# Performance work log

Hardware: AMD Instinct MI355X
Metric: run time of the kernel (lower is better)

Reference implementation:

```python
import jax, jax.numpy as jnp
import numpy as np

N_VOCAB = 50000
V_SUPPORT = 20000
D = 300
H = 512
B = 8192


def setup_inputs() -> dict:
    key = jax.random.key(0)
    ks = jax.random.split(key, 8)
    ws = jax.random.randint(ks[0], (B,), 0, N_VOCAB, dtype=jnp.int64 if jax.config.jax_enable_x64 else jnp.int32)
    cs = jax.random.randint(ks[1], (B,), 0, N_VOCAB, dtype=ws.dtype)
    vectors = jax.random.normal(ks[2], (N_VOCAB, D), dtype=jnp.float32)
    W1 = jax.random.normal(ks[3], (D, H), dtype=jnp.float32) * (1.0 / np.sqrt(D))
    b1 = jnp.zeros((H,), dtype=jnp.float32)
    W2 = jax.random.normal(ks[4], (H, V_SUPPORT), dtype=jnp.float32) * (1.0 / np.sqrt(H))
    b2 = jnp.zeros((V_SUPPORT,), dtype=jnp.float32)
    vector_to_support = jax.random.randint(ks[5], (N_VOCAB,), 0, V_SUPPORT, dtype=ws.dtype)
    return {"ws": ws, "cs": cs, "vectors": vectors, "W1": W1, "b1": b1,
            "W2": W2, "b2": b2, "vector_to_support": vector_to_support}


def reference(ws, cs, vectors, W1, b1, W2, b2, vector_to_support):
    # embedding lookup of context vectors: [B, D]
    v_c = vectors[cs]
    # FeedForward: Linear -> ReLU -> Linear, then LogSoftmax over support
    h = jax.nn.relu(v_c @ W1 + b1)            # [B, H]
    logits = h @ W2 + b2                       # [B, V]
    logp = jax.nn.log_softmax(logits, axis=-1) # [B, V]
    # map target word (vocab index) -> support index, gather per-row logprob.
    # Original does outputs.T[idx].diag() (O(B^2)); the fused equivalent is a
    # per-row gather: logp[arange(B), idx].
    w_sup = vector_to_support[ws]              # [B]
    logprobs = jnp.take_along_axis(logp, w_sup[:, None], axis=-1)[:, 0]
    return -logprobs                            # [B] NLL per example
```

## Files before the change

kernel.cpp:

```cpp
#include <hip/hip_runtime.h>
#include <hip/hip_bf16.h>
#include <hip/hip_fp8.h>
#include <math.h>


typedef __bf16 bf16x8 __attribute__((ext_vector_type(8)));
typedef float f32x4 __attribute__((ext_vector_type(4)));
typedef int i32x4 __attribute__((ext_vector_type(4)));
typedef int i32x8 __attribute__((ext_vector_type(8)));

#define B_N 8192
#define D_N 300
#define K1K 320
#define H_N 512
#define V_N 20000
#define V_PAD 20480
#define NSPLIT 16
#define SPLIT_V 1280
#define NCH 40
#define ROWS_BLK 128
#define CHUNK_BYTES 16384

#define OFF_PART (8388608u)
#define OFF_W1T  (OFF_PART + 16u*8192u*8u)
#define OFF_B2L  (OFF_W1T + 512u*320u*2u)
#define OFF_H8   (OFF_B2L + 20480u*4u)
#define OFF_W2T8 (OFF_H8 + 8192u*512u)

#define SCALE1 0x7F7F7F7F
#define LOG2E  1.4426950408889634f

__device__ inline unsigned short f2bf(float f) {
  __hip_bfloat16 h = __float2bfloat16(f);
  return *reinterpret_cast<unsigned short*>(&h);
}

__device__ inline unsigned char f2fp8(float f) {
  __hip_fp8_e4m3 q(f);
  return (unsigned char)q.__x;
}

__device__ inline unsigned int pk4_fp8(float a, float b, float c, float d) {
#if __has_builtin(__builtin_amdgcn_cvt_pk_fp8_f32)
  int v = 0;
  v = __builtin_amdgcn_cvt_pk_fp8_f32(a, b, v, false);
  v = __builtin_amdgcn_cvt_pk_fp8_f32(c, d, v, true);
  return (unsigned int)v;
#else
  return (unsigned int)f2fp8(a) | ((unsigned int)f2fp8(b) << 8) |
         ((unsigned int)f2fp8(c) << 16) | ((unsigned int)f2fp8(d) << 24);
#endif
}

__device__ inline float fp82f(unsigned char b) {
  __hip_fp8_e4m3 q; q.__x = b;
  return (float)q;
}

__device__ __forceinline__ void gl16(const void* g, void* l) {
  __builtin_amdgcn_global_load_lds(
      (const __attribute__((address_space(1))) void*)g,
      (__attribute__((address_space(3))) void*)l, 16, 0, 0);
}

__global__ __launch_bounds__(256) void kprep(
    const float* __restrict__ W2, unsigned long long* __restrict__ W2T8u,
    const float* __restrict__ W1, unsigned int* __restrict__ W1Tu,
    const float* __restrict__ b2, float* __restrict__ b2l)
{
  __shared__ float tile[64][65];
  const int bid = blockIdx.x;
  const int tid = threadIdx.x;

  if (bid < 2560) {
    const int n0 = (bid >> 3) * 64;
    const int k0 = (bid & 7) * 64;
    #pragma unroll
    for (int it = 0; it < 4; ++it) {
      int idx = it * 256 + tid;
      int i = idx >> 4;
      int j4 = (idx & 15) * 4;
      const float* src = &W2[(size_t)(k0 + i) * V_N + n0 + j4];
      float4 v = make_float4(0.f, 0.f, 0.f, 0.f);
      if (n0 + j4 + 3 < V_N) {
        v = *(const float4*)src;
      } else {
        if (n0 + j4 + 0 < V_N) v.x = src[0];
        if (n0 + j4 + 1 < V_N) v.y = src[1];
        if (n0 + j4 + 2 < V_N) v.z = src[2];
        if (n0 + j4 + 3 < V_N) v.w = src[3];
      }
      tile[i][j4 + 0] = v.x; tile[i][j4 + 1] = v.y;
      tile[i][j4 + 2] = v.z; tile[i][j4 + 3] = v.w;
    }
    __syncthreads();
    #pragma unroll
    for (int it = 0; it < 2; ++it) {
      int idx = it * 256 + tid;
      int nl = idx >> 3;
      int g8 = (idx & 7) * 8;
      int n = n0 + nl;
      unsigned int lo = pk4_fp8(tile[g8 + 0][nl], tile[g8 + 1][nl],
                                tile[g8 + 2][nl], tile[g8 + 3][nl]);
      unsigned int hi = pk4_fp8(tile[g8 + 4][nl], tile[g8 + 5][nl],
                                tile[g8 + 6][nl], tile[g8 + 7][nl]);
      unsigned long long pack = ((unsigned long long)hi << 32) | lo;
      unsigned kk = (unsigned)(k0 + g8);
      unsigned off = ((unsigned)n * 512u + (kk ^ (((unsigned)n & 15u) << 4)));
      W2T8u[off >> 3] = pack;
    }
  } else if (bid < 2600) {
    const int idx0 = bid - 2560;
    const int n0 = (idx0 & 7) * 64;
    const int k0 = (idx0 >> 3) * 64;
    #pragma unroll
    for (int it = 0; it < 16; ++it) {
      int idx = it * 256 + tid;
      int i = idx >> 6;
      int j = idx & 63;
      float v = 0.f;
      if (k0 + i < D_N) v = W1[(size_t)(k0 + i) * H_N + n0 + j];
      tile[i][j] = v;
    }
    __syncthreads();
    #pragma unroll
    for (int it = 0; it < 8; ++it) {
      int idx = it * 256 + tid;
      int nl = idx >> 5;
      int k = (idx & 31) * 2;
      unsigned int lo = f2bf(tile[k][nl]);
      unsigned int hi = f2bf(tile[k + 1][nl]);
      W1Tu[((size_t)(n0 + nl) * K1K + k0 + k) >> 1] = (hi << 16) | lo;
    }
  } else {
    int i = (bid - 2600) * 256 + tid;
    if (i < V_PAD) b2l[i] = (i < V_N) ? b2[i] * LOG2E : -3.0e37f;
  }
}

__global__ __launch_bounds__(256) void k1_hidden(
    const int* __restrict__ cs, const float* __restrict__ vectors,
    const unsigned short* __restrict__ W1T,
    const float* __restrict__ b1, unsigned char* __restrict__ h8Out)
{
  __shared__ __align__(16) unsigned short vca[16][328];
  __shared__ int rowIdx[16];
  const int tid = threadIdx.x;
  const int lane = tid & 63;
  const int w = tid >> 6;
  const int l15 = lane & 15;
  const int l4 = lane >> 4;
  const int r0 = blockIdx.x * 16;
  if (tid < 16) rowIdx[tid] = cs[r0 + tid];
  __syncthreads();
  for (int task = tid; task < 16 * 82; task += 256) {
    const int r = task & 15;
    const int g = task >> 4;
    const int k = g * 4;
    float4 v = make_float4(0.f, 0.f, 0.f, 0.f);
    if (k + 3 < D_N)
      v = *(const float4*)(vectors + (size_t)rowIdx[r] * D_N + k);
    ushort4 pk;
    pk.x = f2bf(v.x); pk.y = f2bf(v.y); pk.z = f2bf(v.z); pk.w = f2bf(v.w);
    *(ushort4*)&vca[r][k] = pk;
  }
  __syncthreads();

  bf16x8 afr[10];
  #pragma unroll
  for (int t = 0; t < 10; ++t)
    afr[t] = *(const bf16x8*)&vca[l15][t * 32 + l4 * 8];

  f32x4 acc[8];
  #pragma unroll
  for (int ct = 0; ct < 8; ++ct) acc[ct] = (f32x4){0.f, 0.f, 0.f, 0.f};

  #pragma unroll
  for (int t = 0; t < 10; ++t) {
    #pragma unroll
    for (int ct = 0; ct < 8; ++ct) {
      const int n = w * 128 + ct * 16 + l15;
      bf16x8 bfr = *(const bf16x8*)(W1T + (size_t)n * K1K + t * 32 + l4 * 8);
      acc[ct] = __builtin_amdgcn_mfma_f32_16x16x32_bf16(afr[t], bfr, acc[ct], 0, 0, 0);
    }
  }

  #pragma unroll
  for (int ct = 0; ct < 8; ++ct) {
    const int n = w * 128 + ct * 16 + l15;
    const float bb = b1[n];
    #pragma unroll
    for (int r = 0; r < 4; ++r) {
      const int row = r0 + l4 * 4 + r;
      h8Out[(size_t)row * H_N + n] = f2fp8(fmaxf(acc[ct][r] + bb, 0.f));
    }
  }
}

__device__ __forceinline__ void stage_chunk(const char* g, char* l, int tid) {
  #pragma unroll
  for (int it = 0; it < 4; ++it) {
    const unsigned o = (unsigned)tid * 16 + it * 4096;
    gl16(g + o, l + o);
  }
}

__global__ __launch_bounds__(256, 4) void k3_fused(
    const unsigned char* __restrict__ h8,
    const char* __restrict__ W2T8,
    const float* __restrict__ b2l,
    float2* __restrict__ partOut)
{
  __shared__ __align__(16) char smB[2 * CHUNK_BYTES];
  __shared__ float b2s[SPLIT_V];
  const int tid = threadIdx.x;
  const int lane = tid & 63;
  const int w = tid >> 6;
  const int l15 = lane & 15;
  const int l4 = lane >> 4;
  const int s = blockIdx.x & 15;
  const int rb = blockIdx.x >> 4;
  const int r0 = rb * ROWS_BLK + w * 32;
  const char* gsplit = W2T8 + (size_t)s * SPLIT_V * 512;
  const int sCol = s * SPLIT_V;
  const int c0 = (rb * 7 + s * 3) % NCH;

  i32x8 afr[2][4];
  #pragma unroll
  for (int m = 0; m < 2; ++m) {
    const unsigned char* ap = h8 + (size_t)(r0 + m * 16 + l15) * H_N + l4 * 32;
    #pragma unroll
    for (int t = 0; t < 4; ++t) {
      i32x4 lo = *(const i32x4*)(ap + t * 128);
      i32x4 hi = *(const i32x4*)(ap + t * 128 + 16);
      afr[m][t] = __builtin_shufflevector(lo, hi, 0, 1, 2, 3, 4, 5, 6, 7);
    }
  }

  float s_run[8];
  #pragma unroll
  for (int ri = 0; ri < 8; ++ri) s_run[ri] = 0.f;

  for (int i = tid; i < SPLIT_V; i += 256) b2s[i] = b2l[sCol + i];

  stage_chunk(gsplit + (size_t)c0 * CHUNK_BYTES, smB, tid);

  const unsigned swz = (unsigned)l15 << 4;

  #pragma unroll 1
  for (int i = 0; i < NCH; ++i) {
    const int cc = (c0 + i >= NCH) ? (c0 + i - NCH) : (c0 + i);
    asm volatile("s_waitcnt vmcnt(0) lgkmcnt(0)" ::: "memory");
    __builtin_amdgcn_s_barrier();

    char* cur = smB + (i & 1) * CHUNK_BYTES;
    if (i + 1 < NCH) {
      const int cn = (cc + 1 >= NCH) ? 0 : (cc + 1);
      stage_chunk(gsplit + (size_t)cn * CHUNK_BYTES,
                  smB + ((i & 1) ^ 1) * CHUNK_BYTES, tid);
    }

    const float b2c0 = b2s[cc * 32 + l15];
    const float b2c1 = b2s[cc * 32 + 16 + l15];

    f32x4 acc[2][2];
    #pragma unroll
    for (int m = 0; m < 2; ++m)
      #pragma unroll
      for (int ct = 0; ct < 2; ++ct) acc[m][ct] = (f32x4){0.f, 0.f, 0.f, 0.f};

    #pragma unroll
    for (int t = 0; t < 4; ++t) {
      const char* bp = cur + l15 * 512;
      i32x4 lo = *(const i32x4*)(bp + (((unsigned)(t * 128 + l4 * 32)) ^ swz));
      i32x4 hi = *(const i32x4*)(bp + (((unsigned)(t * 128 + l4 * 32 + 16)) ^ swz));
      i32x8 bfr = __builtin_shufflevector(lo, hi, 0, 1, 2, 3, 4, 5, 6, 7);
      __builtin_amdgcn_s_setprio(1);
      acc[0][0] = __builtin_amdgcn_mfma_scale_f32_16x16x128_f8f6f4(
          afr[0][t], bfr, acc[0][0], 0, 0, 0, SCALE1, 0, SCALE1);
      acc[1][0] = __builtin_amdgcn_mfma_scale_f32_16x16x128_f8f6f4(
          afr[1][t], bfr, acc[1][0], 0, 0, 0, SCALE1, 0, SCALE1);
      __builtin_amdgcn_s_setprio(0);
    }

    #pragma unroll
    for (int t = 0; t < 4; ++t) {
      const char* bp = cur + (16 + l15) * 512;
      i32x4 lo = *(const i32x4*)(bp + (((unsigned)(t * 128 + l4 * 32)) ^ swz));
      i32x4 hi = *(const i32x4*)(bp + (((unsigned)(t * 128 + l4 * 32 + 16)) ^ swz));
      i32x8 bfr = __builtin_shufflevector(lo, hi, 0, 1, 2, 3, 4, 5, 6, 7);
      __builtin_amdgcn_s_setprio(1);
      acc[0][1] = __builtin_amdgcn_mfma_scale_f32_16x16x128_f8f6f4(
          afr[0][t], bfr, acc[0][1], 0, 0, 0, SCALE1, 0, SCALE1);
      acc[1][1] = __builtin_amdgcn_mfma_scale_f32_16x16x128_f8f6f4(
          afr[1][t], bfr, acc[1][1], 0, 0, 0, SCALE1, 0, SCALE1);
      __builtin_amdgcn_s_setprio(0);
      #pragma unroll
      for (int r2 = 0; r2 < 2; ++r2) {
        const int ri = t * 2 + r2;
        const int m_ = ri >> 2, r_ = ri & 3;
        s_run[ri] += __builtin_amdgcn_exp2f(fmaf(acc[m_][0][r_], LOG2E, b2c0));
      }
    }

    #pragma unroll
    for (int m = 0; m < 2; ++m)
      #pragma unroll
      for (int r = 0; r < 4; ++r)
        s_run[m * 4 + r] += __builtin_amdgcn_exp2f(fmaf(acc[m][1][r], LOG2E, b2c1));
  }

  #pragma unroll
  for (int m = 0; m < 2; ++m)
    #pragma unroll
    for (int r = 0; r < 4; ++r) {
      int ri = m * 4 + r;
      float sc = s_run[ri];
      #pragma unroll
      for (int k = 1; k < 16; k <<= 1) sc += __shfl_xor(sc, k);
      if (l15 == 0) {
        int grow = r0 + m * 16 + l4 * 4 + r;
        partOut[(size_t)s * B_N + grow] = make_float2(0.f, sc);
      }
    }
}

__global__ __launch_bounds__(256) void k45_final(
    const unsigned char* __restrict__ h8, const char* __restrict__ W2T8,
    const float* __restrict__ b2, const int* __restrict__ wsIdx,
    const int* __restrict__ v2s, const float2* __restrict__ part,
    float* __restrict__ out)
{
  const int row = blockIdx.x * 4 + (threadIdx.x >> 6);
  const int lane = threadIdx.x & 63;
  const int tc = v2s[wsIdx[row]];
  unsigned long long hv = *(const unsigned long long*)(h8 + (size_t)row * H_N + lane * 8);
  const unsigned off = ((unsigned)(lane * 8)) ^ (((unsigned)tc & 15u) << 4);
  unsigned long long wv = *(const unsigned long long*)(W2T8 + (size_t)tc * 512 + off);
  float sdot = 0.f;
  #pragma unroll
  for (int j = 0; j < 8; ++j)
    sdot += fp82f((unsigned char)(hv >> (8 * j))) * fp82f((unsigned char)(wv >> (8 * j)));
  #pragma unroll
  for (int k = 32; k >= 1; k >>= 1) sdot += __shfl_xor(sdot, k);
  if (lane == 0) {
    const float tgt = sdot + b2[tc];
    float S = 0.f;
    #pragma unroll
    for (int s = 0; s < NSPLIT; ++s) S += part[(size_t)s * B_N + row].y;
    out[row] = logf(S) - tgt;
  }
}

extern "C" void kernel_launch(void* const* d_in, const int* in_sizes, int n_in,
                              void* d_out, int out_size, void* d_ws, size_t ws_size,
                              hipStream_t stream) {
  const int*   wsIdx   = (const int*)d_in[0];
  const int*   cs      = (const int*)d_in[1];
  const float* vectors = (const float*)d_in[2];
  const float* W1      = (const float*)d_in[3];
  const float* b1      = (const float*)d_in[4];
  const float* W2      = (const float*)d_in[5];
  const float* b2      = (const float*)d_in[6];
  const int*   v2s     = (const int*)d_in[7];

  char* wsb = (char*)d_ws;
  float2* part = (float2*)(wsb + OFF_PART);
  unsigned short* W1T = (unsigned short*)(wsb + OFF_W1T);
  float*  b2l  = (float*)(wsb + OFF_B2L);
  unsigned char* h8   = (unsigned char*)(wsb + OFF_H8);
  char*   W2T8 = wsb + OFF_W2T8;
  float*  out  = (float*)d_out;

  hipLaunchKernelGGL(kprep, dim3(2680), dim3(256), 0, stream,
                     W2, (unsigned long long*)W2T8, W1, (unsigned int*)W1T, b2, b2l);
  hipLaunchKernelGGL(k1_hidden, dim3(B_N / 16), dim3(256), 0, stream, cs, vectors, W1T, b1, h8);
  hipLaunchKernelGGL(k3_fused, dim3((B_N / ROWS_BLK) * NSPLIT), dim3(256), 0, stream,
                     h8, W2T8, b2l, part);
  hipLaunchKernelGGL(k45_final, dim3(B_N / 4), dim3(256), 0, stream,
                     h8, W2T8, b2, wsIdx, v2s, part, out);
}
```

Measured before the change: 117.5 us.

## Load second half of W2 chunk directly from global in MFMA fragment layout

The prep kernel now also writes the second 16 columns of each 32-column W2 chunk into a fragment-ordered buffer, so the fused GEMM can load those B operands straight from global memory into registers. Only the first half of each chunk is staged through LDS, which halves the LDS staging buffer and the LDS traffic. The chunk start rotation per block is dropped. The cost is direct global loads on the critical path with less latency hiding, plus an extra write in prep. The new buffer sits at workspace offset 0, which may overlap other data there.

```diff
diff --git a/kernel.cpp b/kernel.cpp
--- a/kernel.cpp
+++ b/kernel.cpp
@@ -20,7 +20,9 @@
 #define NCH 40
 #define ROWS_BLK 128
 #define CHUNK_BYTES 16384
-
+#define STG_BYTES 8192
+
+#define OFF_W2F  0u
 #define OFF_PART (8388608u)
 #define OFF_W1T  (OFF_PART + 16u*8192u*8u)
 #define OFF_B2L  (OFF_W1T + 512u*320u*2u)
@@ -65,6 +67,7 @@
 
 __global__ __launch_bounds__(256) void kprep(
     const float* __restrict__ W2, unsigned long long* __restrict__ W2T8u,
+    unsigned long long* __restrict__ W2Fu,
     const float* __restrict__ W1, unsigned int* __restrict__ W1Tu,
     const float* __restrict__ b2, float* __restrict__ b2l)
 {
@@ -108,6 +111,14 @@
       unsigned kk = (unsigned)(k0 + g8);
       unsigned off = ((unsigned)n * 512u + (kk ^ (((unsigned)n & 15u) << 4)));
       W2T8u[off >> 3] = pack;
+      if (n & 16) {
+        unsigned sc = (unsigned)n >> 5;
+        unsigned t  = kk >> 7;
+        unsigned l4g = (kk >> 5) & 3;
+        unsigned lanei = l4g * 16 + ((unsigned)n & 15);
+        unsigned foff = (((sc * 4u + t) * 64u) + lanei) * 32u + (kk & 31u);
+        W2Fu[foff >> 3] = pack;
+      }
     }
   } else if (bid < 2600) {
     const int idx0 = bid - 2560;
@@ -197,9 +208,9 @@
   }
 }
 
-__device__ __forceinline__ void stage_chunk(const char* g, char* l, int tid) {
-  #pragma unroll
-  for (int it = 0; it < 4; ++it) {
+__device__ __forceinline__ void stage_half(const char* g, char* l, int tid) {
+  #pragma unroll
+  for (int it = 0; it < 2; ++it) {
     const unsigned o = (unsigned)tid * 16 + it * 4096;
     gl16(g + o, l + o);
   }
@@ -208,10 +219,11 @@
 __global__ __launch_bounds__(256, 4) void k3_fused(
     const unsigned char* __restrict__ h8,
     const char* __restrict__ W2T8,
+    const char* __restrict__ W2F,
     const float* __restrict__ b2l,
     float2* __restrict__ partOut)
 {
-  __shared__ __align__(16) char smB[2 * CHUNK_BYTES];
+  __shared__ __align__(16) char smB[2 * STG_BYTES];
   __shared__ float b2s[SPLIT_V];
   const int tid = threadIdx.x;
   const int lane = tid & 63;
@@ -222,8 +234,8 @@
   const int rb = blockIdx.x >> 4;
   const int r0 = rb * ROWS_BLK + w * 32;
   const char* gsplit = W2T8 + (size_t)s * SPLIT_V * 512;
+  const char* fsplit = W2F + (size_t)s * (NCH * 4 * 2048) + (size_t)lane * 32;
   const int sCol = s * SPLIT_V;
-  const int c0 = (rb * 7 + s * 3) % NCH;
 
   i32x8 afr[2][4];
   #pragma unroll
@@ -243,25 +255,22 @@
 
   for (int i = tid; i < SPLIT_V; i += 256) b2s[i] = b2l[sCol + i];
 
-  stage_chunk(gsplit + (size_t)c0 * CHUNK_BYTES, smB, tid);
+  stage_half(gsplit, smB, tid);
 
   const unsigned swz = (unsigned)l15 << 4;
 
   #pragma unroll 1
-  for (int i = 0; i < NCH; ++i) {
-    const int cc = (c0 + i >= NCH) ? (c0 + i - NCH) : (c0 + i);
+  for (int c = 0; c < NCH; ++c) {
     asm volatile("s_waitcnt vmcnt(0) lgkmcnt(0)" ::: "memory");
     __builtin_amdgcn_s_barrier();
 
-    char* cur = smB + (i & 1) * CHUNK_BYTES;
-    if (i + 1 < NCH) {
-      const int cn = (cc + 1 >= NCH) ? 0 : (cc + 1);
-      stage_chunk(gsplit + (size_t)cn * CHUNK_BYTES,
-                  smB + ((i & 1) ^ 1) * CHUNK_BYTES, tid);
-    }
-
-    const float b2c0 = b2s[cc * 32 + l15];
-    const float b2c1 = b2s[cc * 32 + 16 + l15];
+    char* cur = smB + (c & 1) * STG_BYTES;
+    if (c + 1 < NCH)
+      stage_half(gsplit + (size_t)(c + 1) * CHUNK_BYTES,
+                 smB + ((c & 1) ^ 1) * STG_BYTES, tid);
+
+    const float b2c0 = b2s[c * 32 + l15];
+    const float b2c1 = b2s[c * 32 + 16 + l15];
 
     f32x4 acc[2][2];
     #pragma unroll
@@ -285,9 +294,9 @@
 
     #pragma unroll
     for (int t = 0; t < 4; ++t) {
-      const char* bp = cur + (16 + l15) * 512;
-      i32x4 lo = *(const i32x4*)(bp + (((unsigned)(t * 128 + l4 * 32)) ^ swz));
-      i32x4 hi = *(const i32x4*)(bp + (((unsigned)(t * 128 + l4 * 32 + 16)) ^ swz));
+      const char* fb = fsplit + (size_t)(c * 4 + t) * 2048;
+      i32x4 lo = *(const i32x4*)(fb);
+      i32x4 hi = *(const i32x4*)(fb + 16);
       i32x8 bfr = __builtin_shufflevector(lo, hi, 0, 1, 2, 3, 4, 5, 6, 7);
       __builtin_amdgcn_s_setprio(1);
       acc[0][1] = __builtin_amdgcn_mfma_scale_f32_16x16x128_f8f6f4(
@@ -365,6 +374,7 @@
   const int*   v2s     = (const int*)d_in[7];
 
   char* wsb = (char*)d_ws;
+  char*   W2F  = wsb + OFF_W2F;
   float2* part = (float2*)(wsb + OFF_PART);
   unsigned short* W1T = (unsigned short*)(wsb + OFF_W1T);
   float*  b2l  = (float*)(wsb + OFF_B2L);
@@ -373,10 +383,11 @@
   float*  out  = (float*)d_out;
 
   hipLaunchKernelGGL(kprep, dim3(2680), dim3(256), 0, stream,
-                     W2, (unsigned long long*)W2T8, W1, (unsigned int*)W1T, b2, b2l);
+                     W2, (unsigned long long*)W2T8, (unsigned long long*)W2F,
+                     W1, (unsigned int*)W1T, b2, b2l);
   hipLaunchKernelGGL(k1_hidden, dim3(B_N / 16), dim3(256), 0, stream, cs, vectors, W1T, b1, h8);
   hipLaunchKernelGGL(k3_fused, dim3((B_N / ROWS_BLK) * NSPLIT), dim3(256), 0, stream,
-                     h8, W2T8, b2l, part);
+                     h8, W2T8, W2F, b2l, part);
   hipLaunchKernelGGL(k45_final, dim3(B_N / 4), dim3(256), 0, stream,
                      h8, W2T8, b2, wsIdx, v2s, part, out);
 }
```

Measured after the change: 124.7 us. +6.0%, slower.

## Overlap W2 conversion with hidden-layer compute and unroll chunk loop by two

Applied to the files above, without the earlier changes.

The prep work is split in two. A small kernel converts W1 and b2. A second kernel runs the hidden-layer computation and the large W2 transpose and FP8 pack in the same grid, so the two overlap and one launch boundary goes away. In the main fused kernel, the staggered per-block chunk start is removed and the chunk loop is manually unrolled by two with fixed double-buffer pointers, which drops the modulo and index arithmetic. The risk is that all blocks now read the same W2 chunks in the same order, which could concentrate memory traffic. The merged kernel also uses more shared memory per block.

```diff
diff --git a/kernel.cpp b/kernel.cpp
--- a/kernel.cpp
+++ b/kernel.cpp
@@ -63,18 +63,57 @@
       (__attribute__((address_space(3))) void*)l, 16, 0, 0);
 }
 
-__global__ __launch_bounds__(256) void kprep(
-    const float* __restrict__ W2, unsigned long long* __restrict__ W2T8u,
+__global__ __launch_bounds__(256) void kprep_a(
     const float* __restrict__ W1, unsigned int* __restrict__ W1Tu,
     const float* __restrict__ b2, float* __restrict__ b2l)
 {
   __shared__ float tile[64][65];
   const int bid = blockIdx.x;
   const int tid = threadIdx.x;
-
-  if (bid < 2560) {
-    const int n0 = (bid >> 3) * 64;
-    const int k0 = (bid & 7) * 64;
+  if (bid < 40) {
+    const int n0 = (bid & 7) * 64;
+    const int k0 = (bid >> 3) * 64;
+    #pragma unroll
+    for (int it = 0; it < 16; ++it) {
+      int idx = it * 256 + tid;
+      int i = idx >> 6;
+      int j = idx & 63;
+      float v = 0.f;
+      if (k0 + i < D_N) v = W1[(size_t)(k0 + i) * H_N + n0 + j];
+      tile[i][j] = v;
+    }
+    __syncthreads();
+    #pragma unroll
+    for (int it = 0; it < 8; ++it) {
+      int idx = it * 256 + tid;
+      int nl = idx >> 5;
+      int k = (idx & 31) * 2;
+      unsigned int lo = f2bf(tile[k][nl]);
+      unsigned int hi = f2bf(tile[k + 1][nl]);
+      W1Tu[((size_t)(n0 + nl) * K1K + k0 + k) >> 1] = (hi << 16) | lo;
+    }
+  } else {
+    int i = (bid - 40) * 256 + tid;
+    if (i < V_PAD) b2l[i] = (i < V_N) ? b2[i] * LOG2E : -3.0e37f;
+  }
+}
+
+__global__ __launch_bounds__(256) void kprep_b(
+    const int* __restrict__ cs, const float* __restrict__ vectors,
+    const unsigned short* __restrict__ W1T, const float* __restrict__ b1,
+    unsigned char* __restrict__ h8Out,
+    const float* __restrict__ W2, unsigned long long* __restrict__ W2T8u)
+{
+  __shared__ float tile[64][65];
+  __shared__ __align__(16) unsigned short vca[16][328];
+  __shared__ int rowIdx[16];
+  const int bid = blockIdx.x;
+  const int tid = threadIdx.x;
+
+  if (bid >= 512) {
+    const int wb = bid - 512;
+    const int n0 = (wb >> 3) * 64;
+    const int k0 = (wb & 7) * 64;
     #pragma unroll
     for (int it = 0; it < 4; ++it) {
       int idx = it * 256 + tid;
@@ -109,48 +148,14 @@
       unsigned off = ((unsigned)n * 512u + (kk ^ (((unsigned)n & 15u) << 4)));
       W2T8u[off >> 3] = pack;
     }
-  } else if (bid < 2600) {
-    const int idx0 = bid - 2560;
-    const int n0 = (idx0 & 7) * 64;
-    const int k0 = (idx0 >> 3) * 64;
-    #pragma unroll
-    for (int it = 0; it < 16; ++it) {
-      int idx = it * 256 + tid;
-      int i = idx >> 6;
-      int j = idx & 63;
-      float v = 0.f;
-      if (k0 + i < D_N) v = W1[(size_t)(k0 + i) * H_N + n0 + j];
-      tile[i][j] = v;
-    }
-    __syncthreads();
-    #pragma unroll
-    for (int it = 0; it < 8; ++it) {
-      int idx = it * 256 + tid;
-      int nl = idx >> 5;
-      int k = (idx & 31) * 2;
-      unsigned int lo = f2bf(tile[k][nl]);
-      unsigned int hi = f2bf(tile[k + 1][nl]);
-      W1Tu[((size_t)(n0 + nl) * K1K + k0 + k) >> 1] = (hi << 16) | lo;
-    }
-  } else {
-    int i = (bid - 2600) * 256 + tid;
-    if (i < V_PAD) b2l[i] = (i < V_N) ? b2[i] * LOG2E : -3.0e37f;
-  }
-}
-
-__global__ __launch_bounds__(256) void k1_hidden(
-    const int* __restrict__ cs, const float* __restrict__ vectors,
-    const unsigned short* __restrict__ W1T,
-    const float* __restrict__ b1, unsigned char* __restrict__ h8Out)
-{
-  __shared__ __align__(16) unsigned short vca[16][328];
-  __shared__ int rowIdx[16];
-  const int tid = threadIdx.x;
+    return;
+  }
+
   const int lane = tid & 63;
   const int w = tid >> 6;
   const int l15 = lane & 15;
   const int l4 = lane >> 4;
-  const int r0 = blockIdx.x * 16;
+  const int r0 = bid * 16;
   if (tid < 16) rowIdx[tid] = cs[r0 + tid];
   __syncthreads();
   for (int task = tid; task < 16 * 82; task += 256) {
@@ -204,6 +209,63 @@
     gl16(g + o, l + o);
   }
 }
+
+#define CHUNK_BODY(c, CUR, NXT, GUARD)                                         \
+  {                                                                            \
+    asm volatile("s_waitcnt vmcnt(0) lgkmcnt(0)" ::: "memory");                \
+    __builtin_amdgcn_s_barrier();                                              \
+    if (GUARD)                                                                 \
+      stage_chunk(gsplit + (size_t)((c) + 1) * CHUNK_BYTES, (NXT), tid);       \
+    const float b2c0 = b2s[(c) * 32 + l15];                                    \
+    const float b2c1 = b2s[(c) * 32 + 16 + l15];                               \
+    f32x4 acc[2][2];                                                           \
+    _Pragma("unroll")                                                          \
+    for (int m_ = 0; m_ < 2; ++m_)                                             \
+      _Pragma("unroll")                                                        \
+      for (int ct_ = 0; ct_ < 2; ++ct_)                                        \
+        acc[m_][ct_] = (f32x4){0.f, 0.f, 0.f, 0.f};                            \
+                                                    \
+    _Pragma("unroll")                                                          \
+    for (int t_ = 0; t_ < 4; ++t_) {                                           \
+      const char* bp = (CUR) + l15 * 512;                                      \
+      i32x4 lo = *(const i32x4*)(bp + (((unsigned)(t_*128 + l4*32)) ^ swz));   \
+      i32x4 hi = *(const i32x4*)(bp + (((unsigned)(t_*128 + l4*32 + 16)) ^ swz)); \
+      i32x8 bfr = __builtin_shufflevector(lo, hi, 0, 1, 2, 3, 4, 5, 6, 7);     \
+      __builtin_amdgcn_s_setprio(1);                                           \
+      acc[0][0] = __builtin_amdgcn_mfma_scale_f32_16x16x128_f8f6f4(            \
+          afr[0][t_], bfr, acc[0][0], 0, 0, 0, SCALE1, 0, SCALE1);             \
+      acc[1][0] = __builtin_amdgcn_mfma_scale_f32_16x16x128_f8f6f4(            \
+          afr[1][t_], bfr, acc[1][0], 0, 0, 0, SCALE1, 0, SCALE1);             \
+      __builtin_amdgcn_s_setprio(0);                                           \
+    }                                                                          \
+                          \
+    _Pragma("unroll")                                                          \
+    for (int t_ = 0; t_ < 4; ++t_) {                                           \
+      const char* bp = (CUR) + (16 + l15) * 512;                               \
+      i32x4 lo = *(const i32x4*)(bp + (((unsigned)(t_*128 + l4*32)) ^ swz));   \
+      i32x4 hi = *(const i32x4*)(bp + (((unsigned)(t_*128 + l4*32 + 16)) ^ swz)); \
+      i32x8 bfr = __builtin_shufflevector(lo, hi, 0, 1, 2, 3, 4, 5, 6, 7);     \
+      __builtin_amdgcn_s_setprio(1);                                           \
+      acc[0][1] = __builtin_amdgcn_mfma_scale_f32_16x16x128_f8f6f4(            \
+          afr[0][t_], bfr, acc[0][1], 0, 0, 0, SCALE1, 0, SCALE1);             \
+      acc[1][1] = __builtin_amdgcn_mfma_scale_f32_16x16x128_f8f6f4(            \
+          afr[1][t_], bfr, acc[1][1], 0, 0, 0, SCALE1, 0, SCALE1);             \
+      __builtin_amdgcn_s_setprio(0);                                           \
+      _Pragma("unroll")                                                        \
+      for (int r2_ = 0; r2_ < 2; ++r2_) {                                      \
+        const int ri_ = t_ * 2 + r2_;                                          \
+        const int m_ = ri_ >> 2, r_ = ri_ & 3;                                 \
+        s_run[ri_] += __builtin_amdgcn_exp2f(fmaf(acc[m_][0][r_], LOG2E, b2c0)); \
+      }                                                                        \
+    }                                                                          \
+                                              \
+    _Pragma("unroll")                                                          \
+    for (int m_ = 0; m_ < 2; ++m_)                                             \
+      _Pragma("unroll")                                                        \
+      for (int r_ = 0; r_ < 4; ++r_)                                           \
+        s_run[m_ * 4 + r_] +=                                                  \
+            __builtin_amdgcn_exp2f(fmaf(acc[m_][1][r_], LOG2E, b2c1));         \
+  }
 
 __global__ __launch_bounds__(256, 4) void k3_fused(
     const unsigned char* __restrict__ h8,
@@ -223,7 +285,6 @@
   const int r0 = rb * ROWS_BLK + w * 32;
   const char* gsplit = W2T8 + (size_t)s * SPLIT_V * 512;
   const int sCol = s * SPLIT_V;
-  const int c0 = (rb * 7 + s * 3) % NCH;
 
   i32x8 afr[2][4];
   #pragma unroll
@@ -243,71 +304,16 @@
 
   for (int i = tid; i < SPLIT_V; i += 256) b2s[i] = b2l[sCol + i];
 
-  stage_chunk(gsplit + (size_t)c0 * CHUNK_BYTES, smB, tid);
+  stage_chunk(gsplit, smB, tid);
 
   const unsigned swz = (unsigned)l15 << 4;
+  char* const buf0 = smB;
+  char* const buf1 = smB + CHUNK_BYTES;
 
   #pragma unroll 1
-  for (int i = 0; i < NCH; ++i) {
-    const int cc = (c0 + i >= NCH) ? (c0 + i - NCH) : (c0 + i);
-    asm volatile("s_waitcnt vmcnt(0) lgkmcnt(0)" ::: "memory");
-    __builtin_amdgcn_s_barrier();
-
-    char* cur = smB + (i & 1) * CHUNK_BYTES;
-    if (i + 1 < NCH) {
-      const int cn = (cc + 1 >= NCH) ? 0 : (cc + 1);
-      stage_chunk(gsplit + (size_t)cn * CHUNK_BYTES,
-                  smB + ((i & 1) ^ 1) * CHUNK_BYTES, tid);
-    }
-
-    const float b2c0 = b2s[cc * 32 + l15];
-    const float b2c1 = b2s[cc * 32 + 16 + l15];
-
-    f32x4 acc[2][2];
-    #pragma unroll
-    for (int m = 0; m < 2; ++m)
-      #pragma unroll
-      for (int ct = 0; ct < 2; ++ct) acc[m][ct] = (f32x4){0.f, 0.f, 0.f, 0.f};
-
-    #pragma unroll
-    for (int t = 0; t < 4; ++t) {
-      const char* bp = cur + l15 * 512;
-      i32x4 lo = *(const i32x4*)(bp + (((unsigned)(t * 128 + l4 * 32)) ^ swz));
-      i32x4 hi = *(const i32x4*)(bp + (((unsigned)(t * 128 + l4 * 32 + 16)) ^ swz));
-      i32x8 bfr = __builtin_shufflevector(lo, hi, 0, 1, 2, 3, 4, 5, 6, 7);
-      __builtin_amdgcn_s_setprio(1);
-      acc[0][0] = __builtin_amdgcn_mfma_scale_f32_16x16x128_f8f6f4(
-          afr[0][t], bfr, acc[0][0], 0, 0, 0, SCALE1, 0, SCALE1);
-      acc[1][0] = __builtin_amdgcn_mfma_scale_f32_16x16x128_f8f6f4(
-          afr[1][t], bfr, acc[1][0], 0, 0, 0, SCALE1, 0, SCALE1);
-      __builtin_amdgcn_s_setprio(0);
-    }
-
-    #pragma unroll
-    for (int t = 0; t < 4; ++t) {
-      const char* bp = cur + (16 + l15) * 512;
-      i32x4 lo = *(const i32x4*)(bp + (((unsigned)(t * 128 + l4 * 32)) ^ swz));
-      i32x4 hi = *(const i32x4*)(bp + (((unsigned)(t * 128 + l4 * 32 + 16)) ^ swz));
-      i32x8 bfr = __builtin_shufflevector(lo, hi, 0, 1, 2, 3, 4, 5, 6, 7);
-      __builtin_amdgcn_s_setprio(1);
-      acc[0][1] = __builtin_amdgcn_mfma_scale_f32_16x16x128_f8f6f4(
-          afr[0][t], bfr, acc[0][1], 0, 0, 0, SCALE1, 0, SCALE1);
-      acc[1][1] = __builtin_amdgcn_mfma_scale_f32_16x16x128_f8f6f4(
-          afr[1][t], bfr, acc[1][1], 0, 0, 0, SCALE1, 0, SCALE1);
-      __builtin_amdgcn_s_setprio(0);
-      #pragma unroll
-      for (int r2 = 0; r2 < 2; ++r2) {
-        const int ri = t * 2 + r2;
-        const int m_ = ri >> 2, r_ = ri & 3;
-        s_run[ri] += __builtin_amdgcn_exp2f(fmaf(acc[m_][0][r_], LOG2E, b2c0));
-      }
-    }
-
-    #pragma unroll
-    for (int m = 0; m < 2; ++m)
-      #pragma unroll
-      for (int r = 0; r < 4; ++r)
-        s_run[m * 4 + r] += __builtin_amdgcn_exp2f(fmaf(acc[m][1][r], LOG2E, b2c1));
+  for (int c = 0; c < NCH; c += 2) {
+    CHUNK_BODY(c,     buf0, buf1, true);
+    CHUNK_BODY(c + 1, buf1, buf0, (c + 2 < NCH));
   }
 
   #pragma unroll
@@ -372,9 +378,10 @@
   char*   W2T8 = wsb + OFF_W2T8;
   float*  out  = (float*)d_out;
 
-  hipLaunchKernelGGL(kprep, dim3(2680), dim3(256), 0, stream,
-                     W2, (unsigned long long*)W2T8, W1, (unsigned int*)W1T, b2, b2l);
-  hipLaunchKernelGGL(k1_hidden, dim3(B_N / 16), dim3(256), 0, stream, cs, vectors, W1T, b1, h8);
+  hipLaunchKernelGGL(kprep_a, dim3(120), dim3(256), 0, stream,
+                     W1, (unsigned int*)W1T, b2, b2l);
+  hipLaunchKernelGGL(kprep_b, dim3(512 + 2560), dim3(256), 0, stream,
+                     cs, vectors, W1T, b1, h8, W2, (unsigned long long*)W2T8);
   hipLaunchKernelGGL(k3_fused, dim3((B_N / ROWS_BLK) * NSPLIT), dim3(256), 0, stream,
                      h8, W2T8, b2l, part);
   hipLaunchKernelGGL(k45_final, dim3(B_N / 4), dim3(256), 0, stream,
```

Result: slower. 313.5 us (+166.7%).
